# Kernel tuning notes

Measured on AMD Instinct MI355X. Metric: run time of the kernel, lower is better.

The kernel has to match this reference:

```python
import jax, jax.numpy as jnp
import numpy as np

N_NODES = 50000
N_EDGES = 800000
DIM = 128
N_LAYERS = 2          # num_layers - 1 GIN layers
NUM_GRAPHS = 512      # rows of the sparse graph_pool matrix
BN_EPS = 1e-5


def setup_inputs() -> dict:
    key = jax.random.key(0)
    ks = jax.random.split(key, 10)
    x = jax.random.normal(ks[0], (N_NODES, DIM), dtype=jnp.float32)
    edge_src = jax.random.randint(ks[1], (N_EDGES,), 0, N_NODES, dtype=jnp.int32)
    edge_dst = jax.random.randint(ks[2], (N_EDGES,), 0, N_NODES, dtype=jnp.int32)
    edge_weight = jax.random.uniform(ks[3], (N_EDGES,), dtype=jnp.float32)
    graph_ids = jnp.sort(jax.random.randint(ks[4], (N_NODES,), 0, NUM_GRAPHS, dtype=jnp.int32))
    pool_w = jnp.ones((N_NODES,), dtype=jnp.float32)
    scale = 1.0 / np.sqrt(DIM)
    W1 = jax.random.normal(ks[5], (N_LAYERS, DIM, DIM), dtype=jnp.float32) * scale
    b1 = jnp.zeros((N_LAYERS, DIM), dtype=jnp.float32)
    W2 = jax.random.normal(ks[6], (N_LAYERS, DIM, DIM), dtype=jnp.float32) * scale
    b2 = jnp.zeros((N_LAYERS, DIM), dtype=jnp.float32)
    bn_gamma = jnp.ones((N_LAYERS, DIM), dtype=jnp.float32)
    bn_beta = jnp.zeros((N_LAYERS, DIM), dtype=jnp.float32)
    return {"x": x, "edge_src": edge_src, "edge_dst": edge_dst,
            "edge_weight": edge_weight, "graph_ids": graph_ids, "pool_w": pool_w,
            "W1": W1, "b1": b1, "W2": W2, "b2": b2,
            "bn_gamma": bn_gamma, "bn_beta": bn_beta}


def reference(x, edge_src, edge_dst, edge_weight, graph_ids, pool_w,
              W1, b1, W2, b2, bn_gamma, bn_beta):
    h = x
    n = h.shape[0]
    for l in range(N_LAYERS):
        # pooled = adj @ h, adj in COO form: adj[dst, src] = edge_weight
        msg = edge_weight[:, None] * h[edge_src]                    # [E, D] gather
        pooled = jax.ops.segment_sum(msg, edge_dst, num_segments=n) # [N, D] scatter-add
        # 2-linear MLP (num_mlp_layers=2): Linear -> ReLU -> Linear
        hid = jax.nn.relu(pooled @ W1[l] + b1[l])
        z = hid @ W2[l] + b2[l]
        # BatchNorm1d over the node dimension (training-mode batch stats)
        mu = jnp.mean(z, axis=0)
        var = jnp.mean(jnp.square(z - mu), axis=0)
        z = bn_gamma[l] * (z - mu) * jax.lax.rsqrt(var + BN_EPS) + bn_beta[l]
        h = jax.nn.relu(z)
    x_nodes = h
    # pooled_x = graph_pool @ h, graph_pool[g, i] = pool_w[i] for node i in graph g
    pooled_x = jax.ops.segment_sum(pool_w[:, None] * h, graph_ids,
                                   num_segments=NUM_GRAPHS)
    return pooled_x, x_nodes
```

## Files before the change

### kernel.cpp

```cpp
#include <hip/hip_runtime.h>

#define N_NODES    50000
#define N_EDGES    800000
#define DIM        128
#define NUM_GRAPHS 512
#define BN_EPS     1e-5f

#define NBUCK      196
#define CAP        4608
#define NBINS      2048
#define TILE       4096
#define MLP_ROWS   128
#define POOL_SPLIT 4

typedef unsigned int u32;
typedef unsigned short u16;
typedef __attribute__((ext_vector_type(8))) short bf16x8;
typedef __attribute__((ext_vector_type(4))) float f32x4;

__device__ __forceinline__ u16 f2bf(float f) {
    u32 u = __float_as_uint(f);
    u += 0x7FFF + ((u >> 16) & 1);
    return (u16)(u >> 16);
}
__device__ __forceinline__ float bf2f(u16 h) {
    return __uint_as_float((u32)h << 16);
}

__global__ __launch_bounds__(256)
void fill_zero2_kernel(float* __restrict__ p1, int n1, float* __restrict__ p2, int n2)
{
    int stride = gridDim.x * blockDim.x;
    for (int i = blockIdx.x * 256 + threadIdx.x; i < n1 + n2; i += stride) {
        if (i < n1) p1[i] = 0.f;
        else        p2[i - n1] = 0.f;
    }
}

__global__ __launch_bounds__(256)
void prep_kernel(const float* __restrict__ x, const float* __restrict__ W1,
                 const float* __restrict__ W2, u16* __restrict__ hx,
                 u16* __restrict__ wt)
{
    if (blockIdx.x < 256) {
        int idx = blockIdx.x * 256 + threadIdx.x;
        int m    = idx >> 14;
        int f    = idx & 16383;
        int c    = (f >> 11) & 7;
        int kk   = (f >> 9) & 3;
        int lane = (f >> 3) & 63;
        int e    = f & 7;
        int k = kk * 32 + ((lane >> 4) << 3) + e;
        int j = c * 16 + (lane & 15);
        const float* src = (m & 1) ? W2 : W1;
        src += (m >> 1) * 128 * 128;
        wt[idx] = f2bf(src[k * 128 + j]);
    } else {
        const long long n4 = (long long)N_NODES * DIM / 4;
        long long stride = 1024LL * 256;
        for (long long i = (blockIdx.x - 256) * 256LL + threadIdx.x; i < n4; i += stride) {
            float4 v = ((const float4*)x)[i];
            ushort4 o;
            o.x = f2bf(v.x); o.y = f2bf(v.y); o.z = f2bf(v.z); o.w = f2bf(v.w);
            ((ushort4*)hx)[i] = o;
        }
    }
}

__global__ __launch_bounds__(512)
void partitionA(const int* __restrict__ src, const int* __restrict__ dst,
                const float* __restrict__ ew, int* __restrict__ gCursor,
                uint2* __restrict__ ed2)
{
    __shared__ int cnt[NBUCK];
    __shared__ int off[NBUCK];
    __shared__ int gb[NBUCK];
    __shared__ u32 stg_sw[TILE];
    __shared__ u32 stg_d[TILE];
    __shared__ int scanb[256];

    const int t = threadIdx.x;
    const int base = blockIdx.x * TILE;
    const int tcnt = min(TILE, N_EDGES - base);

    if (t < NBUCK) cnt[t] = 0;
    __syncthreads();

    u32 swv[8], dv[8];
    int rk[8], bk[8];
    #pragma unroll
    for (int j = 0; j < 8; ++j) {
        int e = base + j * 512 + t;
        if (e < N_EDGES) {
            int d = dst[e];
            swv[j] = ((u32)f2bf(ew[e]) << 16) | (u32)src[e];
            dv[j]  = (u32)d;
            bk[j]  = d >> 8;
            rk[j]  = atomicAdd(&cnt[bk[j]], 1);
        } else bk[j] = -1;
    }
    __syncthreads();

    {
        int v = (t < NBUCK) ? cnt[t] : 0;
        if (t < 256) scanb[t] = v;
        __syncthreads();
        for (int o = 1; o < 256; o <<= 1) {
            int x = (t < 256 && t >= o) ? scanb[t - o] : 0;
            __syncthreads();
            if (t < 256) scanb[t] += x;
            __syncthreads();
        }
        if (t < NBUCK) off[t] = scanb[t] - v;
    }
    __syncthreads();

    #pragma unroll
    for (int j = 0; j < 8; ++j) {
        if (bk[j] >= 0) {
            int idx = off[bk[j]] + rk[j];
            stg_sw[idx] = swv[j];
            stg_d[idx]  = dv[j];
        }
    }
    if (t < NBUCK && cnt[t] > 0) gb[t] = atomicAdd(&gCursor[t], cnt[t]);
    __syncthreads();

    for (int j = t; j < tcnt; j += 512) {
        u32 d = stg_d[j];
        int b = (int)(d >> 8);
        long long pos = (long long)b * CAP + gb[b] + (j - off[b]);
        ed2[pos] = make_uint2(stg_sw[j], d);
    }
}

__global__ __launch_bounds__(256)
void partitionB(const uint2* __restrict__ ed2, const int* __restrict__ gCursor,
                int* __restrict__ rowptr, u32* __restrict__ ed)
{
    __shared__ int bstart[256];
    __shared__ int hist[NBINS];
    __shared__ int cursor[NBINS];
    __shared__ int sc[256];

    const int b = blockIdx.x;
    const int t = threadIdx.x;

    {
        int v = (t < NBUCK) ? gCursor[t] : 0;
        sc[t] = v;
        __syncthreads();
        for (int o = 1; o < 256; o <<= 1) {
            int x = (t >= o) ? sc[t - o] : 0;
            __syncthreads();
            sc[t] += x;
            __syncthreads();
        }
        bstart[t] = sc[t] - v;
    }
    __syncthreads();

    const int s0 = bstart[b];
    const int n  = gCursor[b];
    const uint2* srcp = ed2 + (long long)b * CAP;

    #pragma unroll
    for (int q = 0; q < 8; ++q) hist[t + q * 256] = 0;
    __syncthreads();
    for (int j = t; j < n; j += 256) {
        uint2 r = srcp[j];
        int bin = (int)((r.y & 255u) << 3) | (int)((r.x & 0xFFFFu) >> 13);
        atomicAdd(&hist[bin], 1);
    }
    __syncthreads();

    int loc[8]; int sum = 0;
    #pragma unroll
    for (int q = 0; q < 8; ++q) { loc[q] = hist[t * 8 + q]; sum += loc[q]; }
    sc[t] = sum;
    __syncthreads();
    for (int o = 1; o < 256; o <<= 1) {
        int x = (t >= o) ? sc[t - o] : 0;
        __syncthreads();
        sc[t] += x;
        __syncthreads();
    }
    int run = sc[t] - sum;
    rowptr[b * 256 + t] = s0 + run;
    #pragma unroll
    for (int q = 0; q < 8; ++q) {
        cursor[t * 8 + q] = s0 + run;
        run += loc[q];
    }
    __syncthreads();

    for (int j = t; j < n; j += 256) {
        uint2 r = srcp[j];
        int bin = (int)((r.y & 255u) << 3) | (int)((r.x & 0xFFFFu) >> 13);
        int p = atomicAdd(&cursor[bin], 1);
        ed[p] = r.x;
    }
}

template<bool BN>
__global__ __launch_bounds__(256)
void gather_spmm(const u16* __restrict__ h, const u32* __restrict__ ed,
                 const int* __restrict__ rowptr, u16* __restrict__ pooled,
                 const float* __restrict__ stats, const float* __restrict__ gamma,
                 const float* __restrict__ beta)
{
    __shared__ float scs[128];
    __shared__ float shs[128];
    if (BN) {
        if (threadIdx.x < 128) {
            int c = threadIdx.x;
            float mu  = stats[c] * (1.f / N_NODES);
            float var = stats[128 + c] * (1.f / N_NODES) - mu * mu;
            float s   = gamma[c] * rsqrtf(var + BN_EPS);
            scs[c] = s;
            shs[c] = beta[c] - mu * s;
        }
        __syncthreads();
    }

    int node = blockIdx.x * 16 + (threadIdx.x >> 4);
    int lane = threadIdx.x & 15;
    int beg = rowptr[node];
    int end = rowptr[node + 1];

    float sc8[8], sh8[8];
    if (BN) {
        #pragma unroll
        for (int q = 0; q < 8; ++q) {
            sc8[q] = scs[lane * 8 + q];
            sh8[q] = shs[lane * 8 + q];
        }
    }

    float acc[8];
    #pragma unroll
    for (int q = 0; q < 8; ++q) acc[q] = 0.f;

    u32 sw_cur = (beg + lane < end) ? ed[beg + lane] : 0u;
    for (int base = beg; base < end; base += 16) {
        u32 sw_next = (base + 16 + lane < end) ? ed[base + 16 + lane] : 0u;
        int cnt = min(16, end - base);
        #pragma unroll 4
        for (int i = 0; i < cnt; ++i) {
            u32 rec = __shfl(sw_cur, i, 16);
            long long s = (long long)(rec & 0xFFFFu);
            float w = bf2f((u16)(rec >> 16));
            bf16x8 hv = *((const bf16x8*)(h + (s << 7)) + lane);
            #pragma unroll
            for (int q = 0; q < 8; ++q) {
                float v = bf2f((u16)hv[q]);
                if (BN) v = fmaxf(v * sc8[q] + sh8[q], 0.f);
                acc[q] += w * v;
            }
        }
        sw_cur = sw_next;
    }
    bf16x8 o;
    #pragma unroll
    for (int q = 0; q < 8; ++q) o[q] = (short)f2bf(acc[q]);
    *((bf16x8*)(pooled + ((long long)node << 7)) + lane) = o;
}

__global__ __launch_bounds__(512)
void fused_mlp(const u16* __restrict__ A, const u16* __restrict__ wtL,
               const float* __restrict__ b1, const float* __restrict__ b2,
               u16* __restrict__ Z, float* __restrict__ stats)
{
    __shared__ __align__(16) u16 wfrag[32768];
    __shared__ float ssum[128];
    __shared__ float ssq[128];

    const int tid  = threadIdx.x;
    const int lane = tid & 63;
    const int wave = tid >> 6;
    const int l15  = lane & 15;
    const int lk   = lane >> 4;
    const int row0 = blockIdx.x * MLP_ROWS;
    const int wrow = wave * 16;

    #pragma unroll
    for (int i = 0; i < 8; ++i) {
        int idx = tid + i * 512;
        *(bf16x8*)&wfrag[idx * 8] = *(const bf16x8*)(wtL + idx * 8);
    }
    if (tid < 128) { ssum[tid] = 0.f; ssq[tid] = 0.f; }

    bf16x8 afr[4];
    {
        int rg = row0 + wrow + l15;
        bool ok = rg < N_NODES;
        const u16* ap = A + (long long)rg * 128 + lk * 8;
        bf16x8 zero = {};
        #pragma unroll
        for (int kk = 0; kk < 4; ++kk)
            afr[kk] = ok ? *(const bf16x8*)(ap + kk * 32) : zero;
    }
    __syncthreads();

    f32x4 acc1[8];
    #pragma unroll
    for (int c = 0; c < 8; ++c) {
        float bv = b1[c * 16 + l15];
        f32x4 a = {bv, bv, bv, bv};
        #pragma unroll
        for (int kk = 0; kk < 4; ++kk) {
            bf16x8 w = *(bf16x8*)&wfrag[((c * 4 + kk) * 64 + lane) * 8];
            a = __builtin_amdgcn_mfma_f32_16x16x32_bf16(afr[kk], w, a, 0, 0, 0);
        }
        acc1[c] = a;
    }
    __syncthreads();

    #pragma unroll
    for (int c = 0; c < 8; ++c) {
        #pragma unroll
        for (int i = 0; i < 4; ++i) {
            int row = wrow + lk * 4 + i;
            int col = c * 16 + l15;
            wfrag[row * 128 + (col ^ ((row & 15) << 3))] = f2bf(fmaxf(acc1[c][i], 0.f));
        }
    }

    bf16x8 afr2[4];
    {
        int row = wrow + l15;
        #pragma unroll
        for (int kk = 0; kk < 4; ++kk)
            afr2[kk] = *(bf16x8*)&wfrag[row * 128 + ((kk * 32 + lk * 8) ^ ((row & 15) << 3))];
    }

    #pragma unroll
    for (int c = 0; c < 8; ++c) {
        float bv = b2[c * 16 + l15];
        f32x4 a = {bv, bv, bv, bv};
        #pragma unroll
        for (int kk = 0; kk < 4; ++kk) {
            bf16x8 w = *(bf16x8*)&wfrag[16384 + ((c * 4 + kk) * 64 + lane) * 8];
            a = __builtin_amdgcn_mfma_f32_16x16x32_bf16(afr2[kk], w, a, 0, 0, 0);
        }
        float s = 0.f, sq = 0.f;
        #pragma unroll
        for (int i = 0; i < 4; ++i) {
            int row = wrow + lk * 4 + i;
            int rg  = row0 + row;
            float v = a[i];
            bool ok = rg < N_NODES;
            if (ok) { s += v; sq += v * v; }
            wfrag[row * 128 + ((c * 16 + l15) ^ ((row & 15) << 3))] = ok ? f2bf(v) : (u16)0;
        }
        s  += __shfl_xor(s, 16);  s  += __shfl_xor(s, 32);
        sq += __shfl_xor(sq, 16); sq += __shfl_xor(sq, 32);
        if (lk == 0) {
            atomicAdd(&ssum[c * 16 + l15], s);
            atomicAdd(&ssq[c * 16 + l15], sq);
        }
    }

    #pragma unroll
    for (int j = 0; j < 4; ++j) {
        int chunk = j * 64 + lane;
        int rl  = chunk >> 4;
        int c8  = chunk & 15;
        int row = wrow + rl;
        int rg  = row0 + row;
        if (rg < N_NODES) {
            bf16x8 v = *(bf16x8*)&wfrag[row * 128 + ((c8 * 8) ^ ((row & 15) << 3))];
            *(bf16x8*)(Z + (long long)rg * 128 + c8 * 8) = v;
        }
    }
    __syncthreads();
    if (tid < 128) {
        atomicAdd(&stats[tid], ssum[tid]);
        atomicAdd(&stats[128 + tid], ssq[tid]);
    }
}

__global__ __launch_bounds__(256)
void graph_pool_bn(const u16* __restrict__ z, const float* __restrict__ stats,
                   const float* __restrict__ gamma, const float* __restrict__ beta,
                   const int* __restrict__ gid, const float* __restrict__ pw,
                   float* __restrict__ out_nodes, float* __restrict__ out_pool)
{
    __shared__ float scs[128];
    __shared__ float shs[128];
    if (threadIdx.x < 128) {
        int c = threadIdx.x;
        float mu  = stats[c] * (1.f / N_NODES);
        float var = stats[128 + c] * (1.f / N_NODES) - mu * mu;
        float s   = gamma[c] * rsqrtf(var + BN_EPS);
        scs[c] = s;
        shs[c] = beta[c] - mu * s;
    }
    __syncthreads();

    int g    = blockIdx.x >> 2;
    int part = blockIdx.x & 3;

    int lo = 0, hi = N_NODES;
    while (lo < hi) { int m = (lo + hi) >> 1; if (gid[m] < g) lo = m + 1; else hi = m; }
    int start = lo;
    hi = N_NODES;
    while (lo < hi) { int m = (lo + hi) >> 1; if (gid[m] < g + 1) lo = m + 1; else hi = m; }
    int end = lo;

    int len  = end - start;
    int qlen = (len + 3) >> 2;
    int s = start + part * qlen;
    int e = min(end, s + qlen);

    const int t  = threadIdx.x;
    const int rg = t >> 5;
    const int c4 = t & 31;
    float4 sc4 = *(float4*)&scs[c4 * 4];
    float4 sh4 = *(float4*)&shs[c4 * 4];

    float4 acc = make_float4(0.f, 0.f, 0.f, 0.f);
    for (int r = s + rg; r < e; r += 8) {
        float w = pw[r];
        ushort4 hv = *((const ushort4*)(z + (long long)r * DIM) + c4);
        float4 v;
        v.x = fmaxf(bf2f(hv.x) * sc4.x + sh4.x, 0.f);
        v.y = fmaxf(bf2f(hv.y) * sc4.y + sh4.y, 0.f);
        v.z = fmaxf(bf2f(hv.z) * sc4.z + sh4.z, 0.f);
        v.w = fmaxf(bf2f(hv.w) * sc4.w + sh4.w, 0.f);
        *((float4*)(out_nodes + (long long)r * DIM) + c4) = v;
        acc.x += w * v.x; acc.y += w * v.y;
        acc.z += w * v.z; acc.w += w * v.w;
    }

    __shared__ float4 sd[256];
    sd[t] = acc;
    __syncthreads();
    if (t < 32) {
        float4 tot = sd[t];
        #pragma unroll
        for (int i = 1; i < 8; ++i) {
            float4 v = sd[i * 32 + t];
            tot.x += v.x; tot.y += v.y; tot.z += v.z; tot.w += v.w;
        }
        float* op = out_pool + g * DIM + t * 4;
        atomicAdd(op + 0, tot.x);
        atomicAdd(op + 1, tot.y);
        atomicAdd(op + 2, tot.z);
        atomicAdd(op + 3, tot.w);
    }
}

extern "C" void kernel_launch(void* const* d_in, const int* in_sizes, int n_in,
                              void* d_out, int out_size, void* d_ws, size_t ws_size,
                              hipStream_t stream)
{
    const float* x    = (const float*)d_in[0];
    const int*   esrc = (const int*)d_in[1];
    const int*   edst = (const int*)d_in[2];
    const float* ew   = (const float*)d_in[3];
    const int*   gid  = (const int*)d_in[4];
    const float* pw   = (const float*)d_in[5];
    const float* W1   = (const float*)d_in[6];
    const float* b1   = (const float*)d_in[7];
    const float* W2   = (const float*)d_in[8];
    const float* b2   = (const float*)d_in[9];
    const float* gam  = (const float*)d_in[10];
    const float* bet  = (const float*)d_in[11];

    float* out_pool  = (float*)d_out;
    float* out_nodes = (float*)d_out + NUM_GRAPHS * DIM;

    const size_t NF = (size_t)N_NODES * DIM;
    char* w = (char*)d_ws;
    u32*   ed       = (u32*)w;        w += (size_t)N_EDGES * sizeof(u32);
    u16*   pooledBf = (u16*)w;        w += NF * sizeof(u16);
    u16*   zBf      = (u16*)w;        w += NF * sizeof(u16);
    u16*   hx       = (u16*)w;        w += NF * sizeof(u16);
    u16*   wt       = (u16*)w;        w += (size_t)4 * 128 * 128 * sizeof(u16);
    float* stats0   = (float*)w;      w += 256 * sizeof(float);
    float* stats1   = (float*)w;      w += 256 * sizeof(float);
    int*   gCursor  = (int*)w;        w += 256 * sizeof(int);
    int*   rowptr   = (int*)w;        w += (NBUCK * 256 + 64) * sizeof(int);

    uint2* ed2cap   = (uint2*)pooledBf;

    const int mlpGrid    = (N_NODES + MLP_ROWS - 1) / MLP_ROWS;
    const int gatherGrid = (N_NODES + 15) / 16;
    const int partGrid   = (N_EDGES + TILE - 1) / TILE;

    fill_zero2_kernel<<<64, 256, 0, stream>>>(stats0, 768,
                                              out_pool, NUM_GRAPHS * DIM);
    prep_kernel<<<1280, 256, 0, stream>>>(x, W1, W2, hx, wt);
    partitionA<<<partGrid, 512, 0, stream>>>(esrc, edst, ew, gCursor, ed2cap);
    partitionB<<<NBUCK, 256, 0, stream>>>(ed2cap, gCursor, rowptr, ed);

    gather_spmm<false><<<gatherGrid, 256, 0, stream>>>(hx, ed, rowptr, pooledBf,
                                                       nullptr, nullptr, nullptr);
    fused_mlp<<<mlpGrid, 512, 0, stream>>>(pooledBf, wt, b1, b2, zBf, stats0);

    gather_spmm<true><<<gatherGrid, 256, 0, stream>>>(zBf, ed, rowptr, pooledBf,
                                                      stats0, gam, bet);
    fused_mlp<<<mlpGrid, 512, 0, stream>>>(pooledBf, wt + 32768,
                                           b1 + DIM, b2 + DIM, zBf, stats1);

    graph_pool_bn<<<NUM_GRAPHS * POOL_SPLIT, 256, 0, stream>>>(
        zBf, stats1, gam + DIM, bet + DIM, gid, pw, out_nodes, out_pool);
}
```

Baseline: 157.5 us.

## Fold zero-fill into prep, refine edge bins, read MLP weights from global

Merges the zero-fill kernel into prep_kernel as extra blocks, removing one launch. Doubles the per-bucket sort bins in partitionB from 2048 to 4096 so edges are ordered more finely by source within each destination group. fused_mlp stops staging weights in LDS and reads the bf16 weight fragments straight from global or cache, halving LDS use and adding a launch-bounds occupancy hint. The risk is higher latency on the weight loads and extra register pressure in partitionB.

Result: slower. 173.1 us (+9.9%).

```diff
diff --git a/kernel.cpp b/kernel.cpp
--- a/kernel.cpp
+++ b/kernel.cpp
@@ -8,7 +8,7 @@
 
 #define NBUCK      196
 #define CAP        4608
-#define NBINS      2048
+#define NBINS      4096
 #define TILE       4096
 #define MLP_ROWS   128
 #define POOL_SPLIT 4
@@ -28,19 +28,10 @@
 }
 
 __global__ __launch_bounds__(256)
-void fill_zero2_kernel(float* __restrict__ p1, int n1, float* __restrict__ p2, int n2)
-{
-    int stride = gridDim.x * blockDim.x;
-    for (int i = blockIdx.x * 256 + threadIdx.x; i < n1 + n2; i += stride) {
-        if (i < n1) p1[i] = 0.f;
-        else        p2[i - n1] = 0.f;
-    }
-}
-
-__global__ __launch_bounds__(256)
 void prep_kernel(const float* __restrict__ x, const float* __restrict__ W1,
                  const float* __restrict__ W2, u16* __restrict__ hx,
-                 u16* __restrict__ wt)
+                 u16* __restrict__ wt, float* __restrict__ zreg,
+                 float* __restrict__ out_pool)
 {
     if (blockIdx.x < 256) {
         int idx = blockIdx.x * 256 + threadIdx.x;
@@ -55,7 +46,7 @@
         const float* src = (m & 1) ? W2 : W1;
         src += (m >> 1) * 128 * 128;
         wt[idx] = f2bf(src[k * 128 + j]);
-    } else {
+    } else if (blockIdx.x < 1280) {
         const long long n4 = (long long)N_NODES * DIM / 4;
         long long stride = 1024LL * 256;
         for (long long i = (blockIdx.x - 256) * 256LL + threadIdx.x; i < n4; i += stride) {
@@ -63,6 +54,13 @@
             ushort4 o;
             o.x = f2bf(v.x); o.y = f2bf(v.y); o.z = f2bf(v.z); o.w = f2bf(v.w);
             ((ushort4*)hx)[i] = o;
+        }
+    } else {
+        int stride = 64 * 256;
+        for (int i = (blockIdx.x - 1280) * 256 + threadIdx.x;
+             i < 768 + NUM_GRAPHS * DIM; i += stride) {
+            if (i < 768) zreg[i] = 0.f;
+            else         out_pool[i - 768] = 0.f;
         }
     }
 }
@@ -165,18 +163,18 @@
     const uint2* srcp = ed2 + (long long)b * CAP;
 
     #pragma unroll
-    for (int q = 0; q < 8; ++q) hist[t + q * 256] = 0;
+    for (int q = 0; q < 16; ++q) hist[t + q * 256] = 0;
     __syncthreads();
     for (int j = t; j < n; j += 256) {
         uint2 r = srcp[j];
-        int bin = (int)((r.y & 255u) << 3) | (int)((r.x & 0xFFFFu) >> 13);
+        int bin = (int)((r.y & 255u) << 4) | (int)((r.x & 0xFFFFu) >> 12);
         atomicAdd(&hist[bin], 1);
     }
     __syncthreads();
 
-    int loc[8]; int sum = 0;
-    #pragma unroll
-    for (int q = 0; q < 8; ++q) { loc[q] = hist[t * 8 + q]; sum += loc[q]; }
+    int loc[16]; int sum = 0;
+    #pragma unroll
+    for (int q = 0; q < 16; ++q) { loc[q] = hist[t * 16 + q]; sum += loc[q]; }
     sc[t] = sum;
     __syncthreads();
     for (int o = 1; o < 256; o <<= 1) {
@@ -188,15 +186,15 @@
     int run = sc[t] - sum;
     rowptr[b * 256 + t] = s0 + run;
     #pragma unroll
-    for (int q = 0; q < 8; ++q) {
-        cursor[t * 8 + q] = s0 + run;
+    for (int q = 0; q < 16; ++q) {
+        cursor[t * 16 + q] = s0 + run;
         run += loc[q];
     }
     __syncthreads();
 
     for (int j = t; j < n; j += 256) {
         uint2 r = srcp[j];
-        int bin = (int)((r.y & 255u) << 3) | (int)((r.x & 0xFFFFu) >> 13);
+        int bin = (int)((r.y & 255u) << 4) | (int)((r.x & 0xFFFFu) >> 12);
         int p = atomicAdd(&cursor[bin], 1);
         ed[p] = r.x;
     }
@@ -266,12 +264,12 @@
     *((bf16x8*)(pooled + ((long long)node << 7)) + lane) = o;
 }
 
-__global__ __launch_bounds__(512)
+__global__ __launch_bounds__(512, 6)
 void fused_mlp(const u16* __restrict__ A, const u16* __restrict__ wtL,
                const float* __restrict__ b1, const float* __restrict__ b2,
                u16* __restrict__ Z, float* __restrict__ stats)
 {
-    __shared__ __align__(16) u16 wfrag[32768];
+    __shared__ __align__(16) u16 hid[16384];
     __shared__ float ssum[128];
     __shared__ float ssq[128];
 
@@ -283,12 +281,11 @@
     const int row0 = blockIdx.x * MLP_ROWS;
     const int wrow = wave * 16;
 
-    #pragma unroll
-    for (int i = 0; i < 8; ++i) {
-        int idx = tid + i * 512;
-        *(bf16x8*)&wfrag[idx * 8] = *(const bf16x8*)(wtL + idx * 8);
-    }
     if (tid < 128) { ssum[tid] = 0.f; ssq[tid] = 0.f; }
+    __syncthreads();
+
+    const bf16x8* w1g = (const bf16x8*)wtL;
+    const bf16x8* w2g = w1g + 2048;
 
     bf16x8 afr[4];
     {
@@ -300,7 +297,6 @@
         for (int kk = 0; kk < 4; ++kk)
             afr[kk] = ok ? *(const bf16x8*)(ap + kk * 32) : zero;
     }
-    __syncthreads();
 
     f32x4 acc1[8];
     #pragma unroll
@@ -309,12 +305,11 @@
         f32x4 a = {bv, bv, bv, bv};
         #pragma unroll
         for (int kk = 0; kk < 4; ++kk) {
-            bf16x8 w = *(bf16x8*)&wfrag[((c * 4 + kk) * 64 + lane) * 8];
+            bf16x8 w = w1g[(c * 4 + kk) * 64 + lane];
             a = __builtin_amdgcn_mfma_f32_16x16x32_bf16(afr[kk], w, a, 0, 0, 0);
         }
         acc1[c] = a;
     }
-    __syncthreads();
 
     #pragma unroll
     for (int c = 0; c < 8; ++c) {
@@ -322,7 +317,7 @@
         for (int i = 0; i < 4; ++i) {
             int row = wrow + lk * 4 + i;
             int col = c * 16 + l15;
-            wfrag[row * 128 + (col ^ ((row & 15) << 3))] = f2bf(fmaxf(acc1[c][i], 0.f));
+            hid[row * 128 + (col ^ ((row & 15) << 3))] = f2bf(fmaxf(acc1[c][i], 0.f));
         }
     }
 
@@ -331,7 +326,7 @@
         int row = wrow + l15;
         #pragma unroll
         for (int kk = 0; kk < 4; ++kk)
-            afr2[kk] = *(bf16x8*)&wfrag[row * 128 + ((kk * 32 + lk * 8) ^ ((row & 15) << 3))];
+            afr2[kk] = *(bf16x8*)&hid[row * 128 + ((kk * 32 + lk * 8) ^ ((row & 15) << 3))];
     }
 
     #pragma unroll
@@ -340,7 +335,7 @@
         f32x4 a = {bv, bv, bv, bv};
         #pragma unroll
         for (int kk = 0; kk < 4; ++kk) {
-            bf16x8 w = *(bf16x8*)&wfrag[16384 + ((c * 4 + kk) * 64 + lane) * 8];
+            bf16x8 w = w2g[(c * 4 + kk) * 64 + lane];
             a = __builtin_amdgcn_mfma_f32_16x16x32_bf16(afr2[kk], w, a, 0, 0, 0);
         }
         float s = 0.f, sq = 0.f;
@@ -351,7 +346,7 @@
             float v = a[i];
             bool ok = rg < N_NODES;
             if (ok) { s += v; sq += v * v; }
-            wfrag[row * 128 + ((c * 16 + l15) ^ ((row & 15) << 3))] = ok ? f2bf(v) : (u16)0;
+            hid[row * 128 + ((c * 16 + l15) ^ ((row & 15) << 3))] = ok ? f2bf(v) : (u16)0;
         }
         s  += __shfl_xor(s, 16);  s  += __shfl_xor(s, 32);
         sq += __shfl_xor(sq, 16); sq += __shfl_xor(sq, 32);
@@ -369,7 +364,7 @@
         int row = wrow + rl;
         int rg  = row0 + row;
         if (rg < N_NODES) {
-            bf16x8 v = *(bf16x8*)&wfrag[row * 128 + ((c8 * 8) ^ ((row & 15) << 3))];
+            bf16x8 v = *(bf16x8*)&hid[row * 128 + ((c8 * 8) ^ ((row & 15) << 3))];
             *(bf16x8*)(Z + (long long)rg * 128 + c8 * 8) = v;
         }
     }
@@ -489,9 +484,7 @@
     const int gatherGrid = (N_NODES + 15) / 16;
     const int partGrid   = (N_EDGES + TILE - 1) / TILE;
 
-    fill_zero2_kernel<<<64, 256, 0, stream>>>(stats0, 768,
-                                              out_pool, NUM_GRAPHS * DIM);
-    prep_kernel<<<1280, 256, 0, stream>>>(x, W1, W2, hx, wt);
+    prep_kernel<<<1344, 256, 0, stream>>>(x, W1, W2, hx, wt, stats0, out_pool);
     partitionA<<<partGrid, 512, 0, stream>>>(esrc, edst, ew, gCursor, ed2cap);
     partitionB<<<NBUCK, 256, 0, stream>>>(ed2cap, gCursor, rowptr, ed);
 
```
